# Kernel tuning notes

Hardware: AMD Instinct MI355X
Metric: run time of the kernel (lower is better)

## Reference

```python
import jax, jax.numpy as jnp
import numpy as np


def setup_inputs() -> dict:
    key = jax.random.key(0)
    k_u, k_lam, k_B, k_C = jax.random.split(key, 4)
    batch, seq_len, d_model, N = 4, 4096, 1024, 64
    return {
        "u": jax.random.normal(k_u, (batch, seq_len, d_model), dtype=jnp.float32),
        "Lambda": jax.random.normal(k_lam, (N,), dtype=jnp.float32),
        "log_dt": jnp.zeros((1,), dtype=jnp.float32),
        "B": jax.random.normal(k_B, (N, d_model), dtype=jnp.float32),
        "C": jax.random.normal(k_C, (d_model, N), dtype=jnp.float32),
        "D": jnp.zeros((d_model,), dtype=jnp.float32),
    }


def reference(u, Lambda, log_dt, B, C, D):
    # dt = exp(log_dt); A = diag(exp(dt * (-exp(Lambda)))) -> diagonal decay vector a of shape (N,)
    dt = jnp.exp(log_dt)          # (1,)
    a = jnp.exp(-dt * jnp.exp(Lambda))  # (N,)

    # Precompute input projection for all timesteps: Bu[b, t, n] = u[b, t] @ B.T
    Bu = jnp.einsum("bld,nd->bln", u, B)  # (batch, L, N)

    # Sequential diagonal recurrence: x_t = a * x_{t-1} + Bu_t
    def step(x, bu_t):
        x = a * x + bu_t
        return x, x

    x0 = jnp.zeros((u.shape[0], Lambda.shape[0]), dtype=u.dtype)
    _, xs = jax.lax.scan(step, x0, jnp.swapaxes(Bu, 0, 1))  # xs: (L, batch, N)
    xs = jnp.swapaxes(xs, 0, 1)  # (batch, L, N)

    # Output projection + skip: y_t = x_t @ C.T + D * u_t
    return jnp.einsum("bln,dn->bld", xs, C) + D * u
```

## Files before the change

### kernel.cpp

```cpp
#include <hip/hip_runtime.h>
#include <hip/hip_bf16.h>


constexpr int BATCH  = 4;
constexpr int L      = 4096;
constexpr int DM     = 1024;
constexpr int N      = 64;
constexpr int ROWS   = BATCH * L;
constexpr int CHUNK  = 32;
constexpr int NCHUNK = L / CHUNK;

typedef __attribute__((ext_vector_type(8))) short     bf16x8;
typedef __attribute__((ext_vector_type(4))) float     f32x4;

__device__ __forceinline__ unsigned int pk2(float x, float y) {
  __hip_bfloat162 h = __float22bfloat162_rn(make_float2(x, y));
  return *reinterpret_cast<unsigned int*>(&h);
}

__global__ __launch_bounds__(256) void bu_scan(const float* __restrict__ u,
                                               const float* __restrict__ Bm,
                                               const float* __restrict__ Lambda,
                                               const float* __restrict__ log_dt,
                                               unsigned short* __restrict__ xsb,
                                               float* __restrict__ F) {
  __shared__ __align__(16) char smem[27648];
  unsigned short (*As0)[72] = reinterpret_cast<unsigned short (*)[72]>(smem);
  unsigned short (*As1)[72] = reinterpret_cast<unsigned short (*)[72]>(smem + 4608);
  unsigned short (*Bs0)[72] = reinterpret_cast<unsigned short (*)[72]>(smem + 9216);
  unsigned short (*Bs1)[72] = reinterpret_cast<unsigned short (*)[72]>(smem + 18432);
  float (*T)[68] = reinterpret_cast<float (*)[68]>(smem);
  float* W = reinterpret_cast<float*>(smem + 8704);

  const int tid  = threadIdx.x;
  const int lane = tid & 63;
  const int wv   = tid >> 6;
  const int l15  = lane & 15;
  const int g    = lane >> 4;
  const int rh   = wv >> 1;
  const int cp   = wv & 1;
  const int row0 = blockIdx.x * CHUNK;

  const int sra = tid >> 4;
  const int sq  = tid & 15;
  const int srb = tid >> 4;

  f32x4 acc[2] = {};
  float4 pa[2][2], pb[2][4];

  constexpr int NCH = DM / 64;
  #pragma unroll
  for (int s = 0; s < 2; ++s) {
    const int kb = s * 64;
    #pragma unroll
    for (int i = 0; i < 2; ++i)
      pa[s][i] = *reinterpret_cast<const float4*>(
          &u[(long)(row0 + sra + i * 16) * DM + kb + sq * 4]);
    #pragma unroll
    for (int i = 0; i < 4; ++i)
      pb[s][i] = *reinterpret_cast<const float4*>(
          &Bm[(long)(srb + i * 16) * DM + kb + sq * 4]);
  }

  #pragma unroll
  for (int c = 0; c < NCH; ++c) {
    const int s = c & 1;
    unsigned short (*As)[72] = s ? As1 : As0;
    unsigned short (*Bs)[72] = s ? Bs1 : Bs0;
    if (c) __syncthreads();
    #pragma unroll
    for (int i = 0; i < 2; ++i) {
      uint2 ha = {pk2(pa[s][i].x, pa[s][i].y), pk2(pa[s][i].z, pa[s][i].w)};
      *reinterpret_cast<uint2*>(&As[sra + i * 16][sq * 4]) = ha;
    }
    #pragma unroll
    for (int i = 0; i < 4; ++i) {
      uint2 hb = {pk2(pb[s][i].x, pb[s][i].y), pk2(pb[s][i].z, pb[s][i].w)};
      *reinterpret_cast<uint2*>(&Bs[srb + i * 16][sq * 4]) = hb;
    }
    __syncthreads();
    if (c + 2 < NCH) {
      const int kb = (c + 2) * 64;
      #pragma unroll
      for (int i = 0; i < 2; ++i)
        pa[s][i] = *reinterpret_cast<const float4*>(
            &u[(long)(row0 + sra + i * 16) * DM + kb + sq * 4]);
      #pragma unroll
      for (int i = 0; i < 4; ++i)
        pb[s][i] = *reinterpret_cast<const float4*>(
            &Bm[(long)(srb + i * 16) * DM + kb + sq * 4]);
    }
    #pragma unroll
    for (int ks = 0; ks < 2; ++ks) {
      const bf16x8 af = *reinterpret_cast<const bf16x8*>(
          &As[rh * 16 + l15][ks * 32 + g * 8]);
      #pragma unroll
      for (int t = 0; t < 2; ++t) {
        const bf16x8 bfr = *reinterpret_cast<const bf16x8*>(
            &Bs[(cp * 2 + t) * 16 + l15][ks * 32 + g * 8]);
        acc[t] = __builtin_amdgcn_mfma_f32_16x16x32_bf16(af, bfr, acc[t], 0, 0, 0);
      }
    }
  }

  __syncthreads();
  #pragma unroll
  for (int t = 0; t < 2; ++t)
    #pragma unroll
    for (int r = 0; r < 4; ++r)
      T[rh * 16 + g * 4 + r][(cp * 2 + t) * 16 + l15] = acc[t][r];
  __syncthreads();

  const float dtv = __expf(log_dt[0]);
  const float wn  = -dtv * __expf(Lambda[lane]);
  const float a   = __expf(wn);
  const float a8  = __expf(wn * 8.0f);

  float p[8];
  {
    float x = 0.0f;
    #pragma unroll
    for (int j = 0; j < 8; ++j) { x = fmaf(a, x, T[wv * 8 + j][lane]); p[j] = x; }
    W[wv * 64 + lane] = x;
  }
  __syncthreads();
  float P = 0.0f;
  #pragma unroll
  for (int w2 = 0; w2 < 3; ++w2)
    if (w2 < wv) P = fmaf(a8, P, W[w2 * 64 + lane]);
  float cfac = P;
  #pragma unroll
  for (int j = 0; j < 8; ++j) { cfac *= a; T[wv * 8 + j][lane] = p[j] + cfac; }
  if (wv == 3) F[blockIdx.x * N + lane] = p[7] + cfac;
  __syncthreads();

  {
    const int r = tid >> 3, q = tid & 7;
    const float4 v0 = *reinterpret_cast<const float4*>(&T[r][q * 8]);
    const float4 v1 = *reinterpret_cast<const float4*>(&T[r][q * 8 + 4]);
    uint4 o = {pk2(v0.x, v0.y), pk2(v0.z, v0.w), pk2(v1.x, v1.y), pk2(v1.z, v1.w)};
    *reinterpret_cast<uint4*>(&xsb[(long)(row0 + r) * N + q * 8]) = o;
  }
}

__global__ __launch_bounds__(256) void carry_scan(const float* __restrict__ F,
                                                  const float* __restrict__ Lambda,
                                                  const float* __restrict__ log_dt,
                                                  float* __restrict__ carry,
                                                  float* __restrict__ dec) {
  const int t = threadIdx.x;
  const int b = t >> 6;
  const int n = t & 63;
  const float dt = __expf(log_dt[0]);
  const float w  = -dt * __expf(Lambda[n]);
  const float aS = __expf(w * (float)CHUNK);

  #pragma unroll
  for (int i = 0; i < 8; ++i) {
    const int tt = b * 8 + i;
    dec[tt * N + n] = __expf(w * (float)(tt + 1));
  }

  float P = 0.0f;
  #pragma unroll
  for (int h = 0; h < 2; ++h) {
    float f[64];
    #pragma unroll
    for (int c = 0; c < 64; ++c) f[c] = F[(b * NCHUNK + h * 64 + c) * N + n];
    #pragma unroll
    for (int c = 0; c < 64; ++c) {
      carry[(b * NCHUNK + h * 64 + c) * N + n] = P;
      P = fmaf(aS, P, f[c]);
    }
  }
}

__global__ __launch_bounds__(256) void y_gemm(const unsigned short* __restrict__ xsb,
                                              const float* __restrict__ carry,
                                              const float* __restrict__ dec,
                                              const float* __restrict__ Cm,
                                              const float* __restrict__ Dv,
                                              const float* __restrict__ u,
                                              float* __restrict__ y) {
  __shared__ __align__(16) char smem[33792];
  unsigned short (*Xs)[72] = reinterpret_cast<unsigned short (*)[72]>(smem);
  unsigned short (*Cs)[72] = reinterpret_cast<unsigned short (*)[72]>(smem + 9216);
  float (*T)[132] = reinterpret_cast<float (*)[132]>(smem);
  __shared__ float ciS[2][64], Dsh[128];

  const int tid  = threadIdx.x;
  const int lane = tid & 63;
  const int wv   = tid >> 6;
  const int l15  = lane & 15;
  const int g    = lane >> 4;
  const int row0 = (blockIdx.x & 255) * 64;
  const int d0   = (blockIdx.x >> 8) * 128;

  if (tid < 128) ciS[tid >> 6][tid & 63] = carry[((row0 >> 5) + (tid >> 6)) * N + (tid & 63)];
  if (tid < 128) Dsh[tid] = Dv[d0 + tid];
  __syncthreads();

  #pragma unroll
  for (int i = 0; i < 2; ++i) {
    const int idx = tid + i * 256;
    const int r = idx >> 3, q = idx & 7;
    const int h = r >> 5, pos = r & 31;
    const uint4 xv = *reinterpret_cast<const uint4*>(&xsb[(long)(row0 + r) * N + q * 8]);
    const float4 dv0 = *reinterpret_cast<const float4*>(&dec[pos * N + q * 8]);
    const float4 dv1 = *reinterpret_cast<const float4*>(&dec[pos * N + q * 8 + 4]);
    float f[8];
    #pragma unroll
    for (int j = 0; j < 4; ++j) {
      const unsigned int wbits = (&xv.x)[j];
      f[2 * j]     = __uint_as_float(wbits << 16);
      f[2 * j + 1] = __uint_as_float(wbits & 0xFFFF0000u);
    }
    f[0] = fmaf(dv0.x, ciS[h][q * 8 + 0], f[0]);
    f[1] = fmaf(dv0.y, ciS[h][q * 8 + 1], f[1]);
    f[2] = fmaf(dv0.z, ciS[h][q * 8 + 2], f[2]);
    f[3] = fmaf(dv0.w, ciS[h][q * 8 + 3], f[3]);
    f[4] = fmaf(dv1.x, ciS[h][q * 8 + 4], f[4]);
    f[5] = fmaf(dv1.y, ciS[h][q * 8 + 5], f[5]);
    f[6] = fmaf(dv1.z, ciS[h][q * 8 + 6], f[6]);
    f[7] = fmaf(dv1.w, ciS[h][q * 8 + 7], f[7]);
    uint4 o = {pk2(f[0], f[1]), pk2(f[2], f[3]), pk2(f[4], f[5]), pk2(f[6], f[7])};
    *reinterpret_cast<uint4*>(&Xs[r][q * 8]) = o;
  }
  #pragma unroll
  for (int i = 0; i < 8; ++i) {
    const int idx = tid + i * 256;
    const int r = idx >> 4, q = idx & 15;
    const float4 v = *reinterpret_cast<const float4*>(&Cm[(long)(d0 + r) * N + q * 4]);
    uint2 o = {pk2(v.x, v.y), pk2(v.z, v.w)};
    *reinterpret_cast<uint2*>(&Cs[r][q * 4]) = o;
  }
  __syncthreads();

  bf16x8 af[2];
  #pragma unroll
  for (int ks = 0; ks < 2; ++ks)
    af[ks] = *reinterpret_cast<const bf16x8*>(&Xs[wv * 16 + l15][ks * 32 + g * 8]);

  f32x4 acc[8] = {};
  #pragma unroll
  for (int t = 0; t < 8; ++t) {
    #pragma unroll
    for (int ks = 0; ks < 2; ++ks) {
      const bf16x8 bfr = *reinterpret_cast<const bf16x8*>(
          &Cs[t * 16 + l15][ks * 32 + g * 8]);
      acc[t] = __builtin_amdgcn_mfma_f32_16x16x32_bf16(af[ks], bfr, acc[t], 0, 0, 0);
    }
  }

  __syncthreads();
  #pragma unroll
  for (int t = 0; t < 8; ++t)
    #pragma unroll
    for (int r = 0; r < 4; ++r)
      T[wv * 16 + g * 4 + r][t * 16 + l15] = acc[t][r];
  __syncthreads();

  #pragma unroll
  for (int i = 0; i < 8; ++i) {
    const int id = tid + i * 256;
    const int r = id >> 5;
    const int q = id & 31;
    float4 v = *reinterpret_cast<const float4*>(&T[r][q * 4]);
    const float4 dd = *reinterpret_cast<const float4*>(&Dsh[q * 4]);
    if (dd.x != 0.0f || dd.y != 0.0f || dd.z != 0.0f || dd.w != 0.0f) {
      const float4 uu = *reinterpret_cast<const float4*>(
          &u[(long)(row0 + r) * DM + d0 + q * 4]);
      v.x = fmaf(dd.x, uu.x, v.x);
      v.y = fmaf(dd.y, uu.y, v.y);
      v.z = fmaf(dd.z, uu.z, v.z);
      v.w = fmaf(dd.w, uu.w, v.w);
    }
    *reinterpret_cast<float4*>(&y[(long)(row0 + r) * DM + d0 + q * 4]) = v;
  }
}

extern "C" void kernel_launch(void* const* d_in, const int* in_sizes, int n_in,
                              void* d_out, int out_size, void* d_ws, size_t ws_size,
                              hipStream_t stream) {
  const float* u      = (const float*)d_in[0];
  const float* Lambda = (const float*)d_in[1];
  const float* log_dt = (const float*)d_in[2];
  const float* Bm     = (const float*)d_in[3];
  const float* Cm     = (const float*)d_in[4];
  const float* Dv     = (const float*)d_in[5];
  float* y = (float*)d_out;

  const size_t planeB = (size_t)ROWS * N;
  unsigned short* xsb = (unsigned short*)d_ws;
  float* F     = (float*)(xsb + planeB);
  float* carry = F + (size_t)BATCH * NCHUNK * N;
  float* dec   = carry + (size_t)BATCH * NCHUNK * N;

  bu_scan<<<ROWS / CHUNK, 256, 0, stream>>>(u, Bm, Lambda, log_dt, xsb, F);
  carry_scan<<<1, 256, 0, stream>>>(F, Lambda, log_dt, carry, dec);
  y_gemm<<<(ROWS / 64) * (DM / 128), 256, 0, stream>>>(xsb, carry, dec, Cm, Dv, u, y);
}
```

Before: 36.56 us.

## Fuse Bu GEMM, chunk scan, carry propagation and output GEMM into one kernel

```diff
diff --git a/kernel.cpp b/kernel.cpp
--- a/kernel.cpp
+++ b/kernel.cpp
@@ -9,6 +9,7 @@
 constexpr int ROWS   = BATCH * L;
 constexpr int CHUNK  = 32;
 constexpr int NCHUNK = L / CHUNK;
+constexpr int NBLK   = ROWS / CHUNK;
 
 typedef __attribute__((ext_vector_type(8))) short     bf16x8;
 typedef __attribute__((ext_vector_type(4))) float     f32x4;
@@ -18,19 +19,24 @@
   return *reinterpret_cast<unsigned int*>(&h);
 }
 
-__global__ __launch_bounds__(256) void bu_scan(const float* __restrict__ u,
-                                               const float* __restrict__ Bm,
-                                               const float* __restrict__ Lambda,
-                                               const float* __restrict__ log_dt,
-                                               unsigned short* __restrict__ xsb,
-                                               float* __restrict__ F) {
+__global__ __launch_bounds__(256, 2) void fused_s4(const float* __restrict__ u,
+                                                   const float* __restrict__ Bm,
+                                                   const float* __restrict__ Lambda,
+                                                   const float* __restrict__ log_dt,
+                                                   const float* __restrict__ Cm,
+                                                   const float* __restrict__ Dv,
+                                                   float* __restrict__ Fbuf,
+                                                   int* __restrict__ flags,
+                                                   float* __restrict__ y) {
   __shared__ __align__(16) char smem[27648];
   unsigned short (*As0)[72] = reinterpret_cast<unsigned short (*)[72]>(smem);
   unsigned short (*As1)[72] = reinterpret_cast<unsigned short (*)[72]>(smem + 4608);
   unsigned short (*Bs0)[72] = reinterpret_cast<unsigned short (*)[72]>(smem + 9216);
   unsigned short (*Bs1)[72] = reinterpret_cast<unsigned short (*)[72]>(smem + 18432);
   float (*T)[68] = reinterpret_cast<float (*)[68]>(smem);
-  float* W = reinterpret_cast<float*>(smem + 8704);
+  float* W  = reinterpret_cast<float*>(smem + 8704);
+  float* W2 = reinterpret_cast<float*>(smem + 9728);
+  unsigned short (*Xs)[72] = reinterpret_cast<unsigned short (*)[72]>(smem + 10240);
 
   const int tid  = threadIdx.x;
   const int lane = tid & 63;
@@ -39,13 +45,13 @@
   const int g    = lane >> 4;
   const int rh   = wv >> 1;
   const int cp   = wv & 1;
-  const int row0 = blockIdx.x * CHUNK;
+  const int blk  = blockIdx.x;
+  const int row0 = blk * CHUNK;
 
   const int sra = tid >> 4;
   const int sq  = tid & 15;
-  const int srb = tid >> 4;
-
-  f32x4 acc[2] = {};
+
+  f32x4 acc1[2] = {};
   float4 pa[2][2], pb[2][4];
 
   constexpr int NCH = DM / 64;
@@ -59,7 +65,7 @@
     #pragma unroll
     for (int i = 0; i < 4; ++i)
       pb[s][i] = *reinterpret_cast<const float4*>(
-          &Bm[(long)(srb + i * 16) * DM + kb + sq * 4]);
+          &Bm[(long)(sra + i * 16) * DM + kb + sq * 4]);
   }
 
   #pragma unroll
@@ -76,7 +82,7 @@
     #pragma unroll
     for (int i = 0; i < 4; ++i) {
       uint2 hb = {pk2(pb[s][i].x, pb[s][i].y), pk2(pb[s][i].z, pb[s][i].w)};
-      *reinterpret_cast<uint2*>(&Bs[srb + i * 16][sq * 4]) = hb;
+      *reinterpret_cast<uint2*>(&Bs[sra + i * 16][sq * 4]) = hb;
     }
     __syncthreads();
     if (c + 2 < NCH) {
@@ -88,7 +94,7 @@
       #pragma unroll
       for (int i = 0; i < 4; ++i)
         pb[s][i] = *reinterpret_cast<const float4*>(
-            &Bm[(long)(srb + i * 16) * DM + kb + sq * 4]);
+            &Bm[(long)(sra + i * 16) * DM + kb + sq * 4]);
     }
     #pragma unroll
     for (int ks = 0; ks < 2; ++ks) {
@@ -98,7 +104,7 @@
       for (int t = 0; t < 2; ++t) {
         const bf16x8 bfr = *reinterpret_cast<const bf16x8*>(
             &Bs[(cp * 2 + t) * 16 + l15][ks * 32 + g * 8]);
-        acc[t] = __builtin_amdgcn_mfma_f32_16x16x32_bf16(af, bfr, acc[t], 0, 0, 0);
+        acc1[t] = __builtin_amdgcn_mfma_f32_16x16x32_bf16(af, bfr, acc1[t], 0, 0, 0);
       }
     }
   }
@@ -108,13 +114,14 @@
   for (int t = 0; t < 2; ++t)
     #pragma unroll
     for (int r = 0; r < 4; ++r)
-      T[rh * 16 + g * 4 + r][(cp * 2 + t) * 16 + l15] = acc[t][r];
+      T[rh * 16 + g * 4 + r][(cp * 2 + t) * 16 + l15] = acc1[t][r];
   __syncthreads();
 
   const float dtv = __expf(log_dt[0]);
   const float wn  = -dtv * __expf(Lambda[lane]);
   const float a   = __expf(wn);
   const float a8  = __expf(wn * 8.0f);
+  const float aS  = __expf(wn * 32.0f);
 
   float p[8];
   {
@@ -124,158 +131,114 @@
     W[wv * 64 + lane] = x;
   }
   __syncthreads();
-  float P = 0.0f;
-  #pragma unroll
-  for (int w2 = 0; w2 < 3; ++w2)
-    if (w2 < wv) P = fmaf(a8, P, W[w2 * 64 + lane]);
-  float cfac = P;
-  #pragma unroll
-  for (int j = 0; j < 8; ++j) { cfac *= a; T[wv * 8 + j][lane] = p[j] + cfac; }
-  if (wv == 3) F[blockIdx.x * N + lane] = p[7] + cfac;
-  __syncthreads();
-
+  {
+    float P = 0.0f;
+    #pragma unroll
+    for (int w2 = 0; w2 < 3; ++w2)
+      if (w2 < wv) P = fmaf(a8, P, W[w2 * 64 + lane]);
+    float cf = P;
+    #pragma unroll
+    for (int j = 0; j < 8; ++j) { cf *= a; p[j] += cf; }
+  }
+
+  if (wv == 3) {
+    __hip_atomic_store(&Fbuf[blk * 64 + lane], p[7],
+                       __ATOMIC_RELAXED, __HIP_MEMORY_SCOPE_AGENT);
+    __threadfence();
+    if (lane == 0)
+      __hip_atomic_store(&flags[blk], 1, __ATOMIC_RELEASE, __HIP_MEMORY_SCOPE_AGENT);
+  }
+  if (wv == 0) {
+    float carry = 0.0f;
+    const int c = blk & (NCHUNK - 1);
+    if (c) {
+      const int base = blk - c;
+      for (;;) {
+        int f1 = (lane < c) ? __hip_atomic_load(&flags[base + lane],
+                     __ATOMIC_ACQUIRE, __HIP_MEMORY_SCOPE_AGENT) : 1;
+        int f2 = (lane + 64 < c) ? __hip_atomic_load(&flags[base + 64 + lane],
+                     __ATOMIC_ACQUIRE, __HIP_MEMORY_SCOPE_AGENT) : 1;
+        if (__all(f1 != 0 && f2 != 0)) break;
+        __builtin_amdgcn_s_sleep(16);
+      }
+      int j = 0;
+      for (; j + 16 <= c; j += 16) {
+        float fj[16];
+        #pragma unroll
+        for (int k = 0; k < 16; ++k)
+          fj[k] = __hip_atomic_load(&Fbuf[(base + j + k) * 64 + lane],
+                                    __ATOMIC_RELAXED, __HIP_MEMORY_SCOPE_AGENT);
+        #pragma unroll
+        for (int k = 0; k < 16; ++k) carry = fmaf(aS, carry, fj[k]);
+      }
+      for (; j < c; ++j) {
+        const float fj = __hip_atomic_load(&Fbuf[(base + j) * 64 + lane],
+                                           __ATOMIC_RELAXED, __HIP_MEMORY_SCOPE_AGENT);
+        carry = fmaf(aS, carry, fj);
+      }
+    }
+    W2[lane] = carry;
+  }
+  __syncthreads();
+
+  {
+    float tmp = W2[lane];
+    #pragma unroll
+    for (int i = 0; i < 3; ++i) if (i < wv) tmp *= a8;
+    #pragma unroll
+    for (int j = 0; j < 8; ++j) { tmp *= a; T[wv * 8 + j][lane] = p[j] + tmp; }
+  }
+  __syncthreads();
   {
     const int r = tid >> 3, q = tid & 7;
     const float4 v0 = *reinterpret_cast<const float4*>(&T[r][q * 8]);
     const float4 v1 = *reinterpret_cast<const float4*>(&T[r][q * 8 + 4]);
     uint4 o = {pk2(v0.x, v0.y), pk2(v0.z, v0.w), pk2(v1.x, v1.y), pk2(v1.z, v1.w)};
-    *reinterpret_cast<uint4*>(&xsb[(long)(row0 + r) * N + q * 8]) = o;
-  }
-}
-
-__global__ __launch_bounds__(256) void carry_scan(const float* __restrict__ F,
-                                                  const float* __restrict__ Lambda,
-                                                  const float* __restrict__ log_dt,
-                                                  float* __restrict__ carry,
-                                                  float* __restrict__ dec) {
-  const int t = threadIdx.x;
-  const int b = t >> 6;
-  const int n = t & 63;
-  const float dt = __expf(log_dt[0]);
-  const float w  = -dt * __expf(Lambda[n]);
-  const float aS = __expf(w * (float)CHUNK);
-
-  #pragma unroll
-  for (int i = 0; i < 8; ++i) {
-    const int tt = b * 8 + i;
-    dec[tt * N + n] = __expf(w * (float)(tt + 1));
-  }
-
-  float P = 0.0f;
-  #pragma unroll
-  for (int h = 0; h < 2; ++h) {
-    float f[64];
-    #pragma unroll
-    for (int c = 0; c < 64; ++c) f[c] = F[(b * NCHUNK + h * 64 + c) * N + n];
-    #pragma unroll
-    for (int c = 0; c < 64; ++c) {
-      carry[(b * NCHUNK + h * 64 + c) * N + n] = P;
-      P = fmaf(aS, P, f[c]);
-    }
-  }
-}
-
-__global__ __launch_bounds__(256) void y_gemm(const unsigned short* __restrict__ xsb,
-                                              const float* __restrict__ carry,
-                                              const float* __restrict__ dec,
-                                              const float* __restrict__ Cm,
-                                              const float* __restrict__ Dv,
-                                              const float* __restrict__ u,
-                                              float* __restrict__ y) {
-  __shared__ __align__(16) char smem[33792];
-  unsigned short (*Xs)[72] = reinterpret_cast<unsigned short (*)[72]>(smem);
-  unsigned short (*Cs)[72] = reinterpret_cast<unsigned short (*)[72]>(smem + 9216);
-  float (*T)[132] = reinterpret_cast<float (*)[132]>(smem);
-  __shared__ float ciS[2][64], Dsh[128];
-
-  const int tid  = threadIdx.x;
-  const int lane = tid & 63;
-  const int wv   = tid >> 6;
-  const int l15  = lane & 15;
-  const int g    = lane >> 4;
-  const int row0 = (blockIdx.x & 255) * 64;
-  const int d0   = (blockIdx.x >> 8) * 128;
-
-  if (tid < 128) ciS[tid >> 6][tid & 63] = carry[((row0 >> 5) + (tid >> 6)) * N + (tid & 63)];
-  if (tid < 128) Dsh[tid] = Dv[d0 + tid];
-  __syncthreads();
-
-  #pragma unroll
-  for (int i = 0; i < 2; ++i) {
-    const int idx = tid + i * 256;
-    const int r = idx >> 3, q = idx & 7;
-    const int h = r >> 5, pos = r & 31;
-    const uint4 xv = *reinterpret_cast<const uint4*>(&xsb[(long)(row0 + r) * N + q * 8]);
-    const float4 dv0 = *reinterpret_cast<const float4*>(&dec[pos * N + q * 8]);
-    const float4 dv1 = *reinterpret_cast<const float4*>(&dec[pos * N + q * 8 + 4]);
-    float f[8];
-    #pragma unroll
-    for (int j = 0; j < 4; ++j) {
-      const unsigned int wbits = (&xv.x)[j];
-      f[2 * j]     = __uint_as_float(wbits << 16);
-      f[2 * j + 1] = __uint_as_float(wbits & 0xFFFF0000u);
-    }
-    f[0] = fmaf(dv0.x, ciS[h][q * 8 + 0], f[0]);
-    f[1] = fmaf(dv0.y, ciS[h][q * 8 + 1], f[1]);
-    f[2] = fmaf(dv0.z, ciS[h][q * 8 + 2], f[2]);
-    f[3] = fmaf(dv0.w, ciS[h][q * 8 + 3], f[3]);
-    f[4] = fmaf(dv1.x, ciS[h][q * 8 + 4], f[4]);
-    f[5] = fmaf(dv1.y, ciS[h][q * 8 + 5], f[5]);
-    f[6] = fmaf(dv1.z, ciS[h][q * 8 + 6], f[6]);
-    f[7] = fmaf(dv1.w, ciS[h][q * 8 + 7], f[7]);
-    uint4 o = {pk2(f[0], f[1]), pk2(f[2], f[3]), pk2(f[4], f[5]), pk2(f[6], f[7])};
     *reinterpret_cast<uint4*>(&Xs[r][q * 8]) = o;
   }
-  #pragma unroll
-  for (int i = 0; i < 8; ++i) {
-    const int idx = tid + i * 256;
-    const int r = idx >> 4, q = idx & 15;
-    const float4 v = *reinterpret_cast<const float4*>(&Cm[(long)(d0 + r) * N + q * 4]);
-    uint2 o = {pk2(v.x, v.y), pk2(v.z, v.w)};
-    *reinterpret_cast<uint2*>(&Cs[r][q * 4]) = o;
-  }
-  __syncthreads();
-
-  bf16x8 af[2];
-  #pragma unroll
-  for (int ks = 0; ks < 2; ++ks)
-    af[ks] = *reinterpret_cast<const bf16x8*>(&Xs[wv * 16 + l15][ks * 32 + g * 8]);
-
-  f32x4 acc[8] = {};
-  #pragma unroll
-  for (int t = 0; t < 8; ++t) {
-    #pragma unroll
-    for (int ks = 0; ks < 2; ++ks) {
-      const bf16x8 bfr = *reinterpret_cast<const bf16x8*>(
-          &Cs[t * 16 + l15][ks * 32 + g * 8]);
-      acc[t] = __builtin_amdgcn_mfma_f32_16x16x32_bf16(af[ks], bfr, acc[t], 0, 0, 0);
-    }
-  }
-
-  __syncthreads();
-  #pragma unroll
-  for (int t = 0; t < 8; ++t)
-    #pragma unroll
-    for (int r = 0; r < 4; ++r)
-      T[wv * 16 + g * 4 + r][t * 16 + l15] = acc[t][r];
-  __syncthreads();
-
-  #pragma unroll
-  for (int i = 0; i < 8; ++i) {
-    const int id = tid + i * 256;
-    const int r = id >> 5;
-    const int q = id & 31;
-    float4 v = *reinterpret_cast<const float4*>(&T[r][q * 4]);
-    const float4 dd = *reinterpret_cast<const float4*>(&Dsh[q * 4]);
-    if (dd.x != 0.0f || dd.y != 0.0f || dd.z != 0.0f || dd.w != 0.0f) {
-      const float4 uu = *reinterpret_cast<const float4*>(
-          &u[(long)(row0 + r) * DM + d0 + q * 4]);
-      v.x = fmaf(dd.x, uu.x, v.x);
-      v.y = fmaf(dd.y, uu.y, v.y);
-      v.z = fmaf(dd.z, uu.z, v.z);
-      v.w = fmaf(dd.w, uu.w, v.w);
-    }
-    *reinterpret_cast<float4*>(&y[(long)(row0 + r) * DM + d0 + q * 4]) = v;
+  __syncthreads();
+
+  const int d0w = wv * 256;
+  bf16x8 af2[2][2];
+  #pragma unroll
+  for (int m = 0; m < 2; ++m)
+    #pragma unroll
+    for (int ks = 0; ks < 2; ++ks)
+      af2[m][ks] = *reinterpret_cast<const bf16x8*>(&Xs[m * 16 + l15][ks * 32 + g * 8]);
+
+  #pragma unroll
+  for (int t = 0; t < 16; ++t) {
+    const long crow = (long)(d0w + t * 16 + l15) * N;
+    const float4 c00 = *reinterpret_cast<const float4*>(&Cm[crow + g * 8]);
+    const float4 c01 = *reinterpret_cast<const float4*>(&Cm[crow + g * 8 + 4]);
+    const float4 c10 = *reinterpret_cast<const float4*>(&Cm[crow + 32 + g * 8]);
+    const float4 c11 = *reinterpret_cast<const float4*>(&Cm[crow + 32 + g * 8 + 4]);
+    uint4 w0 = {pk2(c00.x, c00.y), pk2(c00.z, c00.w), pk2(c01.x, c01.y), pk2(c01.z, c01.w)};
+    uint4 w1 = {pk2(c10.x, c10.y), pk2(c10.z, c10.w), pk2(c11.x, c11.y), pk2(c11.z, c11.w)};
+    const bf16x8 bf0 = *reinterpret_cast<const bf16x8*>(&w0);
+    const bf16x8 bf1 = *reinterpret_cast<const bf16x8*>(&w1);
+    f32x4 a0 = {}, a1 = {};
+    a0 = __builtin_amdgcn_mfma_f32_16x16x32_bf16(af2[0][0], bf0, a0, 0, 0, 0);
+    a0 = __builtin_amdgcn_mfma_f32_16x16x32_bf16(af2[0][1], bf1, a0, 0, 0, 0);
+    a1 = __builtin_amdgcn_mfma_f32_16x16x32_bf16(af2[1][0], bf0, a1, 0, 0, 0);
+    a1 = __builtin_amdgcn_mfma_f32_16x16x32_bf16(af2[1][1], bf1, a1, 0, 0, 0);
+
+    const int col = d0w + t * 16 + l15;
+    const float dD = Dv[col];
+    #pragma unroll
+    for (int r = 0; r < 4; ++r) {
+      const long row = row0 + g * 4 + r;
+      float v = a0[r];
+      if (dD != 0.0f) v = fmaf(dD, u[row * DM + col], v);
+      y[row * DM + col] = v;
+    }
+    #pragma unroll
+    for (int r = 0; r < 4; ++r) {
+      const long row = row0 + 16 + g * 4 + r;
+      float v = a1[r];
+      if (dD != 0.0f) v = fmaf(dD, u[row * DM + col], v);
+      y[row * DM + col] = v;
+    }
   }
 }
 
@@ -290,13 +253,9 @@
   const float* Dv     = (const float*)d_in[5];
   float* y = (float*)d_out;
 
-  const size_t planeB = (size_t)ROWS * N;
-  unsigned short* xsb = (unsigned short*)d_ws;
-  float* F     = (float*)(xsb + planeB);
-  float* carry = F + (size_t)BATCH * NCHUNK * N;
-  float* dec   = carry + (size_t)BATCH * NCHUNK * N;
-
-  bu_scan<<<ROWS / CHUNK, 256, 0, stream>>>(u, Bm, Lambda, log_dt, xsb, F);
-  carry_scan<<<1, 256, 0, stream>>>(F, Lambda, log_dt, carry, dec);
-  y_gemm<<<(ROWS / 64) * (DM / 128), 256, 0, stream>>>(xsb, carry, dec, Cm, Dv, u, y);
+  float* Fbuf = (float*)d_ws;
+  int*   flags = (int*)(Fbuf + (size_t)NBLK * N);
+
+  hipMemsetAsync(flags, 0, NBLK * sizeof(int), stream);
+  fused_s4<<<NBLK, 256, 0, stream>>>(u, Bm, Lambda, log_dt, Cm, Dv, Fbuf, flags, y);
 }
```

After: 75.06 us. 2.05x slower.
